# Optimization experiments

Hardware: AMD Instinct MI355X
Metric: run time of the kernel (lower is better)

The kernel has to match this reference:

```python
import jax, jax.numpy as jnp
import numpy as np

DEPTH = 4
CHUNK = 16


def tp(a, b):
    """Graded tensor (outer) product on flattened levels: (...,m)x(...,n)->(...,m*n)."""
    return jnp.einsum('...i,...j->...ij', a, b).reshape(*a.shape[:-1], a.shape[-1] * b.shape[-1])


def ta_mul(a, b):
    """Truncated tensor-algebra product of two group-like elements (implicit level-0 == 1).
    a, b: lists of levels 1..D, level k flattened to C**k."""
    out = []
    for k in range(len(a)):
        t = a[k] + b[k]
        for i in range(k):
            t = t + tp(a[i], b[k - 1 - i])
        out.append(t)
    return out


def ta_mulz(a, b):
    """Product when both elements have level-0 == 0."""
    out = []
    for k in range(len(a)):
        t = jnp.zeros_like(a[k])
        for i in range(k):
            t = t + tp(a[i], b[k - 1 - i])
        out.append(t)
    return out


def ta_exp(a):
    """exp of a level-0-free element, truncated at DEPTH; returns levels 1..D (level-0 == 1 implicit)."""
    out = list(a)
    p = a
    fact = 1.0
    for m in range(2, len(a) + 1):
        p = ta_mulz(a, p)
        fact *= m
        out = [o + q / fact for o, q in zip(out, p)]
    return out


def ta_log(s):
    """Truncated log of group-like element g = 1 + s; input s = levels 1..D of g."""
    out = list(s)
    p = s
    sign = 1.0
    for m in range(2, len(s) + 1):
        p = ta_mulz(s, p)
        sign = -sign
        out = [o + (sign / m) * q for o, q in zip(out, p)]
    return out


def bch(a, b):
    """BCH merge: log(exp(a) (x) exp(b)) in the truncated algebra."""
    return ta_log(ta_mul(ta_exp(a), ta_exp(b)))


def exp_l1(d):
    """exp of a pure level-1 element d (shape (...,C)): level k = d^(x)k / k!."""
    levels = [d]
    cur = d
    fact = 1.0
    for k in range(2, DEPTH + 1):
        cur = tp(cur, d)
        fact *= k
        levels.append(cur / fact)
    return levels


def chunk_signatures(inc):
    """inc: (B, N, L, C) per-chunk increments -> signature levels [(B,N,C), (B,N,C^2), ...]
    via Chen: sig = exp(d_1) (x) ... (x) exp(d_L)."""
    carry0 = tuple(exp_l1(inc[:, :, 0]))
    xs = jnp.moveaxis(inc[:, :, 1:], 2, 0)  # (L-1, B, N, C)
    def step(carry, d):
        return tuple(ta_mul(list(carry), exp_l1(d))), None
    carry, _ = jax.lax.scan(step, carry0, xs)
    return list(carry)


def hillis_steele(levels):
    """Inclusive associative scan over chunk dim (axis=1) with BCH merge.
    bch(0, b) == b exactly, so zero-padding handles the boundary."""
    N = levels[0].shape[1]
    pref = levels
    d = 1
    while d < N:
        shifted = [jnp.concatenate([jnp.zeros_like(l[:, :d]), l[:, :-d]], axis=1) for l in pref]
        pref = bch(shifted, pref)
        d *= 2
    return pref


def _forward(x, W1, b1, W2, b2):
    B, T, Cin = x.shape
    t = jnp.linspace(0.0, 1.0, T, dtype=x.dtype)
    path = jnp.concatenate([x, jnp.broadcast_to(t[None, :, None], (B, T, 1)).astype(x.dtype)], axis=-1)
    C = Cin + 1
    # basepoint=True: path starts at 0, so increments are diff of [0; path]
    inc = jnp.diff(path, axis=1, prepend=jnp.zeros((B, 1, C), x.dtype))
    N = T // CHUNK
    inc = inc.reshape(B, N, CHUNK, C)
    sig = chunk_signatures(inc)          # levels 1..D, (B,N,C^k)
    logl = ta_log(sig)                   # truncated log-signature per chunk
    pref = hillis_steele(logl)           # inclusive BCH prefix scan
    flat = jnp.concatenate(pref, axis=-1)  # (B, N, mem_dim)
    pooled = flat.mean(axis=1)           # readout_pool == 'mean'
    h = jnp.maximum(pooled @ W1 + b1, 0.0)
    return h @ W2 + b2


def setup_inputs() -> dict:
    key = jax.random.key(0)
    k0, k1, k2 = jax.random.split(key, 3)
    B, T, Cin = 8, 2048, 7
    mem_dim, H, out_dim = 4680, 256, 1
    x = jax.random.normal(k0, (B, T, Cin), dtype=jnp.float32)
    W1 = jax.random.normal(k1, (mem_dim, H), dtype=jnp.float32) * (1.0 / np.sqrt(mem_dim))
    b1 = jnp.zeros((H,), jnp.float32)
    W2 = jax.random.normal(k2, (H, out_dim), dtype=jnp.float32) * (1.0 / np.sqrt(H))
    b2 = jnp.zeros((out_dim,), jnp.float32)
    return {"x": x, "W1": W1, "b1": b1, "W2": W2, "b2": b2}


def reference(x, W1, b1, W2, b2):
    return _forward(x, W1, b1, W2, b2)
```

## Files before the change

kernel.cpp:

```cpp
#include <hip/hip_runtime.h>


#define MEM   4680
#define OFF2  8
#define OFF3  72
#define OFF4  584
#define NCH   128
#define NG    32
#define LCH   4
#define TLEN  2048
#define GSTR  20
#define ZN    (8 * MEM + 8 * 256)

__global__ __launch_bounds__(256) void group_sig_kernel(const float* __restrict__ x,
                                                        float* __restrict__ Q,
                                                        float* __restrict__ zbuf) {
    int blk = blockIdx.x;
    int b = blk >> 5, g = blk & 31;
    int tid = threadIdx.x;
    int lane = tid & 63, w = tid >> 6;
    int kq = lane >> 3, lq = lane & 7;

    for (int i = blk * 256 + tid; i < ZN; i += 256 * 256) zbuf[i] = 0.0f;

    __shared__ float sInc[64 * 8];
    __shared__ __attribute__((aligned(16))) float sG[512 * GSTR];
    __shared__ float sA[MEM];
    __shared__ float loc3[512];
    __shared__ float loc2[64];
    __shared__ float loc1[8];

    for (int e = tid; e < 64 * 8; e += 256) {
        int s = e >> 3, c = e & 7;
        int t = g * 64 + s;
        float v;
        if (c < 7) {
            float cur  = x[(b * TLEN + t) * 7 + c];
            float prev = (t > 0) ? x[(b * TLEN + t - 1) * 7 + c] : 0.0f;
            v = cur - prev;
        } else {
            v = (t > 0) ? (1.0f / 2047.0f) : 0.0f;
        }
        sInc[e] = v;
    }
    for (int m = tid; m < MEM; m += 256) sA[m] = 0.0f;
    __syncthreads();

    for (int c = 0; c < LCH; c++) {
        const float* dch = &sInc[c * 128];

        int pos1 = tid, pos2 = tid + 256;
        int i1 = pos1 >> 6, j1 = (pos1 >> 3) & 7, k1 = pos1 & 7;
        int i2 = pos2 >> 6;
        float p1a = 0.0f, l2a = 0.0f, l3a = 0.0f;
        float p1b = 0.0f, l2b = 0.0f, l3b = 0.0f;
        float ga[16], gb[16];
#pragma unroll
        for (int t = 0; t < 16; t++) {
            float di1 = dch[t * 8 + i1], di2 = dch[t * 8 + i2];
            float dj = dch[t * 8 + j1], dk = dch[t * 8 + k1];
            ga[t] = l3a + dk * (l2a * 0.5f + dj * (p1a * (1.0f / 6.0f) + di1 * (1.0f / 24.0f)));
            gb[t] = l3b + dk * (l2b * 0.5f + dj * (p1b * (1.0f / 6.0f) + di2 * (1.0f / 24.0f)));
            l3a += dk * (l2a + dj * (p1a * 0.5f + di1 * (1.0f / 6.0f)));
            l3b += dk * (l2b + dj * (p1b * 0.5f + di2 * (1.0f / 6.0f)));
            l2a += p1a * dj + di1 * dj * 0.5f;
            l2b += p1b * dj + di2 * dj * 0.5f;
            p1a += di1;
            p1b += di2;
        }
        {
            float4* gp1 = (float4*)&sG[pos1 * GSTR];
            float4* gp2 = (float4*)&sG[pos2 * GSTR];
            gp1[0] = make_float4(ga[0], ga[1], ga[2], ga[3]);
            gp1[1] = make_float4(ga[4], ga[5], ga[6], ga[7]);
            gp1[2] = make_float4(ga[8], ga[9], ga[10], ga[11]);
            gp1[3] = make_float4(ga[12], ga[13], ga[14], ga[15]);
            gp2[0] = make_float4(gb[0], gb[1], gb[2], gb[3]);
            gp2[1] = make_float4(gb[4], gb[5], gb[6], gb[7]);
            gp2[2] = make_float4(gb[8], gb[9], gb[10], gb[11]);
            gp2[3] = make_float4(gb[12], gb[13], gb[14], gb[15]);
        }
        loc3[pos1] = l3a;
        loc3[pos2] = l3b;
        if (k1 == 0) { loc2[pos1 >> 3] = l2a; loc2[pos2 >> 3] = l2b; }
        if ((pos1 & 63) == 0) { loc1[i1] = p1a; loc1[i2] = p1b; }
        __syncthreads();

        float dl[16];
#pragma unroll
        for (int t = 0; t < 16; t++) dl[t] = dch[t * 8 + lq];

        float r4[16];
#pragma unroll
        for (int r = 0; r < 16; r++) {
            int row = w + 4 * r;
            int i = row >> 3, j = row & 7;
            int m = row * 64 + lane;
            const float4* gp = (const float4*)&sG[(row * 8 + kq) * GSTR];
            float4 g0 = gp[0], g1 = gp[1], g2 = gp[2], g3 = gp[3];
            float acc = g0.x * dl[0] + g0.y * dl[1] + g0.z * dl[2] + g0.w * dl[3]
                      + g1.x * dl[4] + g1.y * dl[5] + g1.z * dl[6] + g1.w * dl[7]
                      + g2.x * dl[8] + g2.y * dl[9] + g2.z * dl[10] + g2.w * dl[11]
                      + g3.x * dl[12] + g3.y * dl[13] + g3.z * dl[14] + g3.w * dl[15];
            r4[r] = sA[OFF4 + m] + acc
                  + sA[i] * loc3[j * 64 + lane]
                  + sA[OFF2 + row] * loc2[lane]
                  + sA[OFF3 + row * 8 + kq] * loc1[lq];
        }
        float r3[2];
#pragma unroll
        for (int q = 0; q < 2; q++) {
            int m3 = tid + 256 * q;
            float l3v = (q == 0) ? l3a : l3b;
            r3[q] = sA[OFF3 + m3] + l3v
                  + sA[m3 >> 6] * loc2[m3 & 63]
                  + sA[OFF2 + (m3 >> 3)] * loc1[m3 & 7];
        }
        float r2v = 0.0f, r1v = 0.0f;
        if (tid < 64) r2v = sA[OFF2 + tid] + loc2[tid] + sA[tid >> 3] * loc1[tid & 7];
        if (tid < 8)  r1v = sA[tid] + loc1[tid];
        __syncthreads();

        size_t qbase = (size_t)(blk * LCH + c) * MEM;
#pragma unroll
        for (int r = 0; r < 16; r++) {
            int row = w + 4 * r;
            int m = row * 64 + lane;
            sA[OFF4 + m] = r4[r];
            Q[qbase + OFF4 + m] = r4[r];
        }
        sA[OFF3 + tid] = r3[0];       Q[qbase + OFF3 + tid] = r3[0];
        sA[OFF3 + 256 + tid] = r3[1]; Q[qbase + OFF3 + 256 + tid] = r3[1];
        if (tid < 64) { sA[OFF2 + tid] = r2v; Q[qbase + OFF2 + tid] = r2v; }
        if (tid < 8)  { sA[tid] = r1v;        Q[qbase + tid] = r1v; }
        __syncthreads();
    }
}

__global__ __launch_bounds__(256) void scan_fused_kernel(const float* __restrict__ Q,
                                                         float* __restrict__ P) {
    int bx = blockIdx.x;
    int b = bx >> 4, s = bx & 15;
    int tid = threadIdx.x;

    __shared__ float st1[NG][8];
    __shared__ float st2[NG][64];
    __shared__ float st3[NG][32];
    __shared__ float sp1[NG][8];
    __shared__ float sp2[NG][64];
    __shared__ float sp3[NG][32];

    {
        int g = tid >> 3, i = tid & 7;
        st1[g][i] = Q[((size_t)((b * NG + g) * LCH + 3)) * MEM + i];
    }
    for (int m = tid; m < NG * 64; m += 256) {
        int g = m >> 6, e = m & 63;
        st2[g][e] = Q[((size_t)((b * NG + g) * LCH + 3)) * MEM + OFF2 + e];
    }
    for (int m = tid; m < NG * 32; m += 256) {
        int g = m >> 5, e = m & 31;
        st3[g][e] = Q[((size_t)((b * NG + g) * LCH + 3)) * MEM + OFF3 + s * 32 + e];
    }
    __syncthreads();

    if (tid < 64) {
        int i = tid >> 3, k = tid & 7;
        float p1acc = 0.0f, p2acc = 0.0f;
        for (int g = 0; g < NG; g++) {
            sp2[g][tid] = p2acc;
            if (k == 0) sp1[g][i] = p1acc;
            if (s == 0) {
                size_t prow = (size_t)(b * NG + g) * MEM;
                P[prow + OFF2 + tid] = p2acc;
                if (k == 0) P[prow + i] = p1acc;
            }
            p2acc += st2[g][tid] + p1acc * st1[g][k];
            p1acc += st1[g][i];
        }
    }
    __syncthreads();

    if (tid < 32) {
        int ijk = s * 32 + tid;
        int i = ijk >> 6, jk = ijk & 63, ij = ijk >> 3, k = ijk & 7;
        float acc3 = 0.0f;
        for (int g = 0; g < NG; g++) {
            sp3[g][tid] = acc3;
            P[(size_t)(b * NG + g) * MEM + OFF3 + ijk] = acc3;
            acc3 += st3[g][tid] + sp1[g][i] * st2[g][jk] + sp2[g][ij] * st1[g][k];
        }
    }
    __syncthreads();

    int m = s * 256 + tid;
    int i = m >> 9, jkl = m & 511, ij = m >> 6, ijk_l = tid >> 3, kl = m & 63, l = m & 7;
    float acc4 = 0.0f;
#pragma unroll 4
    for (int g = 0; g < NG; g++) {
        size_t prow = (size_t)(b * NG + g) * MEM;
        size_t qrow = (size_t)((b * NG + g) * LCH + 3) * MEM;
        P[prow + OFF4 + m] = acc4;
        acc4 += Q[qrow + OFF4 + m]
              + sp1[g][i] * Q[qrow + OFF3 + jkl]
              + sp2[g][ij] * st2[g][kl]
              + sp3[g][ijk_l] * st1[g][l];
    }
}

__global__ __launch_bounds__(256) void apply_log_pool_kernel(const float* __restrict__ Q,
                                                             const float* __restrict__ P,
                                                             float* __restrict__ pooled) {
    int blk = blockIdx.x;
    int b = blk >> 5;
    int tid = threadIdx.x;
    int lane = tid & 63, w = tid >> 6;
    int kq = lane >> 3, lq = lane & 7;

    __shared__ float sA[MEM];
    __shared__ float sB[LCH * MEM];
    __shared__ float sR[OFF4];
    __shared__ float sP23[512];

    {
        const float4* srcP = (const float4*)(P + (size_t)blk * MEM);
        float4* dstA = (float4*)sA;
        for (int m = tid; m < MEM / 4; m += 256) dstA[m] = srcP[m];
        const float4* srcQ = (const float4*)(Q + (size_t)blk * LCH * MEM);
        float4* dstB = (float4*)sB;
        for (int m = tid; m < LCH * MEM / 4; m += 256) dstB[m] = srcQ[m];
    }
    __syncthreads();

    float pool4[16];
#pragma unroll
    for (int r = 0; r < 16; r++) pool4[r] = 0.0f;
    float pool3[2] = {0.0f, 0.0f};
    float pool2 = 0.0f, pool1 = 0.0f;

    for (int c = 0; c < LCH; c++) {
        const float* sBc = &sB[c * MEM];
        float b1l = sBc[lq];
        float b2lane = sBc[OFF2 + lane];

        float r1 = 0.0f, r2v = 0.0f;
        float r3v[2];
#pragma unroll
        for (int q = 0; q < 2; q++) {
            int m3 = tid + 256 * q;
            r3v[q] = sA[OFF3 + m3] + sBc[OFF3 + m3]
                   + sA[m3 >> 6] * sBc[OFF2 + (m3 & 63)]
                   + sA[OFF2 + (m3 >> 3)] * sBc[m3 & 7];
        }
        if (tid < 64) r2v = sA[OFF2 + tid] + sBc[OFF2 + tid] + sA[tid >> 3] * sBc[tid & 7];
        if (tid < 8)  r1 = sA[tid] + sBc[tid];

        float r4[16];
#pragma unroll
        for (int r = 0; r < 16; r++) {
            int row = w + 4 * r;
            int i = row >> 3, j = row & 7;
            int m = row * 64 + lane;
            r4[r] = sA[OFF4 + m] + sBc[OFF4 + m]
                  + sA[i] * sBc[OFF3 + j * 64 + lane]
                  + sA[OFF2 + row] * b2lane
                  + sA[OFF3 + row * 8 + kq] * b1l;
        }

        __syncthreads();
#pragma unroll
        for (int q = 0; q < 2; q++) sR[OFF3 + tid + 256 * q] = r3v[q];
        if (tid < 64) sR[OFF2 + tid] = r2v;
        if (tid < 8)  sR[tid] = r1;
        __syncthreads();

#pragma unroll
        for (int q = 0; q < 2; q++) {
            int m3 = tid + 256 * q;
            int i = m3 >> 6;
            sP23[m3] = sR[i] * sR[OFF2 + (m3 & 63)]
                     + sR[OFF2 + i * 8 + ((m3 >> 3) & 7)] * sR[m3 & 7];
        }
        __syncthreads();

        float s1l = sR[lq];
        float s2lane = sR[OFF2 + lane];
        float p22lane = sR[kq] * sR[lq];
#pragma unroll
        for (int r = 0; r < 16; r++) {
            int row = w + 4 * r;
            int i = row >> 3, j = row & 7;
            float s1i = sR[i];
            float p24 = s1i * sR[OFF3 + j * 64 + lane] + sR[OFF2 + row] * s2lane
                      + sR[OFF3 + row * 8 + kq] * s1l;
            float p34 = s1i * sP23[j * 64 + lane] + sR[OFF2 + row] * p22lane;
            float p44 = s1i * sR[j] * p22lane;
            pool4[r] += r4[r] - 0.5f * p24 + (1.0f / 3.0f) * p34 - 0.25f * p44;
        }
#pragma unroll
        for (int q = 0; q < 2; q++) {
            int m3 = tid + 256 * q;
            int i3 = m3 >> 6;
            pool3[q] += r3v[q] - 0.5f * sP23[m3] + (1.0f / 3.0f) * sR[i3] * p22lane;
        }
        if (tid < 64) pool2 += r2v - 0.5f * sR[tid >> 3] * sR[tid & 7];
        if (tid < 8)  pool1 += r1;
    }

    const float sc = 1.0f / (float)NCH;
    float* pb = pooled + (size_t)b * MEM;
#pragma unroll
    for (int r = 0; r < 16; r++) {
        int row = w + 4 * r;
        atomicAdd(&pb[OFF4 + row * 64 + lane], pool4[r] * sc);
    }
    atomicAdd(&pb[OFF3 + tid], pool3[0] * sc);
    atomicAdd(&pb[OFF3 + 256 + tid], pool3[1] * sc);
    if (tid < 64) atomicAdd(&pb[OFF2 + tid], pool2 * sc);
    if (tid < 8)  atomicAdd(&pb[tid], pool1 * sc);
}

__global__ __launch_bounds__(256) void gemv1_kernel(const float* __restrict__ pooled,
                                                    const float* __restrict__ W1,
                                                    float* __restrict__ hbuf) {
    int kc = blockIdx.x;
    int tid = threadIdx.x;
    int k0 = kc * 32;
    __shared__ float sp[8][32];
    {
        int b = tid >> 5, kk = tid & 31;
        sp[b][kk] = (k0 + kk < MEM) ? pooled[b * MEM + k0 + kk] : 0.0f;
    }
    __syncthreads();
    float acc[8];
#pragma unroll
    for (int b = 0; b < 8; b++) acc[b] = 0.0f;
    int kend = (k0 + 32 < MEM) ? (k0 + 32) : MEM;
    for (int k = k0; k < kend; k++) {
        float wv = W1[(size_t)k * 256 + tid];
#pragma unroll
        for (int b = 0; b < 8; b++) acc[b] += sp[b][k - k0] * wv;
    }
#pragma unroll
    for (int b = 0; b < 8; b++) atomicAdd(&hbuf[b * 256 + tid], acc[b]);
}

__global__ __launch_bounds__(256) void final_kernel(const float* __restrict__ hbuf,
                                                    const float* __restrict__ b1,
                                                    const float* __restrict__ W2,
                                                    const float* __restrict__ b2,
                                                    float* __restrict__ outp) {
    int b = blockIdx.x;
    int tid = threadIdx.x;
    float v = hbuf[b * 256 + tid] + b1[tid];
    v = fmaxf(v, 0.0f) * W2[tid];
    __shared__ float sRed[256];
    sRed[tid] = v;
    __syncthreads();
    for (int s = 128; s > 0; s >>= 1) {
        if (tid < s) sRed[tid] += sRed[tid + s];
        __syncthreads();
    }
    if (tid == 0) outp[b] = sRed[0] + b2[0];
}

extern "C" void kernel_launch(void* const* d_in, const int* in_sizes, int n_in,
                              void* d_out, int out_size, void* d_ws, size_t ws_size,
                              hipStream_t stream) {
    const float* x  = (const float*)d_in[0];
    const float* W1 = (const float*)d_in[1];
    const float* b1 = (const float*)d_in[2];
    const float* W2 = (const float*)d_in[3];
    const float* b2 = (const float*)d_in[4];
    float* out = (float*)d_out;

    float* ws = (float*)d_ws;
    float* Q      = ws;
    float* P      = Q + (size_t)1024 * MEM;
    float* pooled = P + (size_t)256 * MEM;
    float* hbuf   = pooled + 8 * MEM;

    group_sig_kernel<<<256, 256, 0, stream>>>(x, Q, pooled);
    scan_fused_kernel<<<128, 256, 0, stream>>>(Q, P);
    apply_log_pool_kernel<<<256, 256, 0, stream>>>(Q, P, pooled);
    gemv1_kernel<<<147, 256, 0, stream>>>(pooled, W1, hbuf);
    final_kernel<<<8, 256, 0, stream>>>(hbuf, b1, W2, b2, out);
}
```

Before: 127.5 us.

## Recompute per-chunk signatures in pool kernel instead of storing all to global

The first kernel now writes only the group-total signature per 64-step group instead of all four intermediate chunk prefix signatures, which shrinks the workspace traffic. The apply/pool kernel reloads the increments and recomputes the chunk prefix signatures on the fly. Level-4 accumulation is also restructured so each thread owns 8 contiguous l-entries, with running sums over l in registers and no staged G buffer in shared memory. This trades duplicated signature compute for fewer global writes and reads.

```diff
diff --git a/kernel.cpp b/kernel.cpp
--- a/kernel.cpp
+++ b/kernel.cpp
@@ -2,142 +2,106 @@
 
 
 #define MEM   4680
-#define OFF2  8
-#define OFF3  72
-#define OFF4  584
-#define NCH   128
+#define L2OFF 8
+#define L3OFF 72
+#define L4OFF 584
 #define NG    32
-#define LCH   4
 #define TLEN  2048
-#define GSTR  20
 #define ZN    (8 * MEM + 8 * 256)
 
-__global__ __launch_bounds__(256) void group_sig_kernel(const float* __restrict__ x,
-                                                        float* __restrict__ Q,
-                                                        float* __restrict__ zbuf) {
-    int blk = blockIdx.x;
-    int b = blk >> 5, g = blk & 31;
-    int tid = threadIdx.x;
-    int lane = tid & 63, w = tid >> 6;
-    int kq = lane >> 3, lq = lane & 7;
-
-    for (int i = blk * 256 + tid; i < ZN; i += 256 * 256) zbuf[i] = 0.0f;
-
-    __shared__ float sInc[64 * 8];
-    __shared__ __attribute__((aligned(16))) float sG[512 * GSTR];
-    __shared__ float sA[MEM];
-    __shared__ float loc3[512];
-    __shared__ float loc2[64];
-    __shared__ float loc1[8];
-
-    for (int e = tid; e < 64 * 8; e += 256) {
+__device__ __forceinline__ void load_inc(const float* __restrict__ x, int b, int g,
+                                         float* sInc, int tid) {
+    for (int e = tid; e < 512; e += 256) {
         int s = e >> 3, c = e & 7;
         int t = g * 64 + s;
         float v;
         if (c < 7) {
             float cur  = x[(b * TLEN + t) * 7 + c];
-            float prev = (t > 0) ? x[(b * TLEN + t - 1) * 7 + c] : 0.0f;
+            float prev = (t > 0) ? x[(b * TLEN + t - 1) * 7 + c] : 0.f;
             v = cur - prev;
-        } else {
-            v = (t > 0) ? (1.0f / 2047.0f) : 0.0f;
-        }
+        } else v = (t > 0) ? (1.f / 2047.f) : 0.f;
         sInc[e] = v;
     }
-    for (int m = tid; m < MEM; m += 256) sA[m] = 0.0f;
-    __syncthreads();
-
-    for (int c = 0; c < LCH; c++) {
-        const float* dch = &sInc[c * 128];
-
-        int pos1 = tid, pos2 = tid + 256;
-        int i1 = pos1 >> 6, j1 = (pos1 >> 3) & 7, k1 = pos1 & 7;
-        int i2 = pos2 >> 6;
-        float p1a = 0.0f, l2a = 0.0f, l3a = 0.0f;
-        float p1b = 0.0f, l2b = 0.0f, l3b = 0.0f;
-        float ga[16], gb[16];
-#pragma unroll
-        for (int t = 0; t < 16; t++) {
-            float di1 = dch[t * 8 + i1], di2 = dch[t * 8 + i2];
-            float dj = dch[t * 8 + j1], dk = dch[t * 8 + k1];
-            ga[t] = l3a + dk * (l2a * 0.5f + dj * (p1a * (1.0f / 6.0f) + di1 * (1.0f / 24.0f)));
-            gb[t] = l3b + dk * (l2b * 0.5f + dj * (p1b * (1.0f / 6.0f) + di2 * (1.0f / 24.0f)));
-            l3a += dk * (l2a + dj * (p1a * 0.5f + di1 * (1.0f / 6.0f)));
-            l3b += dk * (l2b + dj * (p1b * 0.5f + di2 * (1.0f / 6.0f)));
-            l2a += p1a * dj + di1 * dj * 0.5f;
-            l2b += p1b * dj + di2 * dj * 0.5f;
-            p1a += di1;
-            p1b += di2;
-        }
-        {
-            float4* gp1 = (float4*)&sG[pos1 * GSTR];
-            float4* gp2 = (float4*)&sG[pos2 * GSTR];
-            gp1[0] = make_float4(ga[0], ga[1], ga[2], ga[3]);
-            gp1[1] = make_float4(ga[4], ga[5], ga[6], ga[7]);
-            gp1[2] = make_float4(ga[8], ga[9], ga[10], ga[11]);
-            gp1[3] = make_float4(ga[12], ga[13], ga[14], ga[15]);
-            gp2[0] = make_float4(gb[0], gb[1], gb[2], gb[3]);
-            gp2[1] = make_float4(gb[4], gb[5], gb[6], gb[7]);
-            gp2[2] = make_float4(gb[8], gb[9], gb[10], gb[11]);
-            gp2[3] = make_float4(gb[12], gb[13], gb[14], gb[15]);
-        }
-        loc3[pos1] = l3a;
-        loc3[pos2] = l3b;
-        if (k1 == 0) { loc2[pos1 >> 3] = l2a; loc2[pos2 >> 3] = l2b; }
-        if ((pos1 & 63) == 0) { loc1[i1] = p1a; loc1[i2] = p1b; }
-        __syncthreads();
-
-        float dl[16];
-#pragma unroll
-        for (int t = 0; t < 16; t++) dl[t] = dch[t * 8 + lq];
-
-        float r4[16];
-#pragma unroll
-        for (int r = 0; r < 16; r++) {
-            int row = w + 4 * r;
-            int i = row >> 3, j = row & 7;
-            int m = row * 64 + lane;
-            const float4* gp = (const float4*)&sG[(row * 8 + kq) * GSTR];
-            float4 g0 = gp[0], g1 = gp[1], g2 = gp[2], g3 = gp[3];
-            float acc = g0.x * dl[0] + g0.y * dl[1] + g0.z * dl[2] + g0.w * dl[3]
-                      + g1.x * dl[4] + g1.y * dl[5] + g1.z * dl[6] + g1.w * dl[7]
-                      + g2.x * dl[8] + g2.y * dl[9] + g2.z * dl[10] + g2.w * dl[11]
-                      + g3.x * dl[12] + g3.y * dl[13] + g3.z * dl[14] + g3.w * dl[15];
-            r4[r] = sA[OFF4 + m] + acc
-                  + sA[i] * loc3[j * 64 + lane]
-                  + sA[OFF2 + row] * loc2[lane]
-                  + sA[OFF3 + row * 8 + kq] * loc1[lq];
-        }
-        float r3[2];
-#pragma unroll
-        for (int q = 0; q < 2; q++) {
-            int m3 = tid + 256 * q;
-            float l3v = (q == 0) ? l3a : l3b;
-            r3[q] = sA[OFF3 + m3] + l3v
-                  + sA[m3 >> 6] * loc2[m3 & 63]
-                  + sA[OFF2 + (m3 >> 3)] * loc1[m3 & 7];
-        }
-        float r2v = 0.0f, r1v = 0.0f;
-        if (tid < 64) r2v = sA[OFF2 + tid] + loc2[tid] + sA[tid >> 3] * loc1[tid & 7];
-        if (tid < 8)  r1v = sA[tid] + loc1[tid];
-        __syncthreads();
-
-        size_t qbase = (size_t)(blk * LCH + c) * MEM;
-#pragma unroll
-        for (int r = 0; r < 16; r++) {
-            int row = w + 4 * r;
-            int m = row * 64 + lane;
-            sA[OFF4 + m] = r4[r];
-            Q[qbase + OFF4 + m] = r4[r];
-        }
-        sA[OFF3 + tid] = r3[0];       Q[qbase + OFF3 + tid] = r3[0];
-        sA[OFF3 + 256 + tid] = r3[1]; Q[qbase + OFF3 + 256 + tid] = r3[1];
-        if (tid < 64) { sA[OFF2 + tid] = r2v; Q[qbase + OFF2 + tid] = r2v; }
-        if (tid < 8)  { sA[tid] = r1v;        Q[qbase + tid] = r1v; }
-        __syncthreads();
-    }
-}
-
-__global__ __launch_bounds__(256) void scan_fused_kernel(const float* __restrict__ Q,
+}
+
+__device__ __forceinline__ void chunk_step(const float* dch, float* sA, float* U, int tid) {
+    float* loc3 = U;
+    float* loc2 = U + 512;
+    float* loc1 = U + 576;
+    const int i1 = tid >> 6, j1 = (tid >> 3) & 7, k1 = tid & 7;
+    const int pos2 = tid + 256, i2 = pos2 >> 6;
+    float p1a = 0.f, l2a = 0.f, l3a = 0.f, p1b = 0.f, l2b = 0.f, l3b = 0.f;
+    float Sa[8], Sb[8];
+#pragma unroll
+    for (int l = 0; l < 8; l++) { Sa[l] = 0.f; Sb[l] = 0.f; }
+#pragma unroll
+    for (int t = 0; t < 16; t++) {
+        const float* dr = dch + t * 8;
+        float di1 = dr[i1], di2 = dr[i2], dj = dr[j1], dk = dr[k1];
+        float ga = l3a + dk * (l2a * 0.5f + dj * (p1a * (1.f/6.f) + di1 * (1.f/24.f)));
+        float gb = l3b + dk * (l2b * 0.5f + dj * (p1b * (1.f/6.f) + di2 * (1.f/24.f)));
+#pragma unroll
+        for (int l = 0; l < 8; l++) { float dv = dr[l]; Sa[l] += ga * dv; Sb[l] += gb * dv; }
+        l3a += dk * (l2a + dj * (p1a * 0.5f + di1 * (1.f/6.f)));
+        l3b += dk * (l2b + dj * (p1b * 0.5f + di2 * (1.f/6.f)));
+        l2a += (p1a + di1 * 0.5f) * dj;
+        l2b += (p1b + di2 * 0.5f) * dj;
+        p1a += di1; p1b += di2;
+    }
+    loc3[tid] = l3a; loc3[pos2] = l3b;
+    if (k1 == 0) { loc2[tid >> 3] = l2a; loc2[(tid >> 3) + 32] = l2b; }
+    if ((tid & 63) == 0) { loc1[i1] = p1a; loc1[i2] = p1b; }
+    __syncthreads();
+    float n4a[8], n4b[8];
+    {
+        float a1 = sA[i1], a2 = sA[L2OFF + (tid >> 3)], a3 = sA[L3OFF + tid];
+        float c1_ = sA[i2], c2_ = sA[L2OFF + (tid >> 3) + 32], c3_ = sA[L3OFF + pos2];
+        const float* l3p = &loc3[(tid & 63) * 8];
+        const float* l2p = &loc2[k1 * 8];
+#pragma unroll
+        for (int l = 0; l < 8; l++) {
+            float v3 = l3p[l], v2 = l2p[l], v1 = loc1[l];
+            n4a[l] = sA[L4OFF + tid * 8 + l]  + Sa[l] + a1 * v3 + a2 * v2 + a3 * v1;
+            n4b[l] = sA[L4OFF + pos2 * 8 + l] + Sb[l] + c1_ * v3 + c2_ * v2 + c3_ * v1;
+        }
+    }
+    float n3a = sA[L3OFF + tid]  + l3a + sA[i1] * loc2[tid & 63] + sA[L2OFF + (tid >> 3)] * loc1[k1];
+    float n3b = sA[L3OFF + pos2] + l3b + sA[i2] * loc2[tid & 63] + sA[L2OFF + (tid >> 3) + 32] * loc1[k1];
+    float n2v = 0.f, n1v = 0.f;
+    if (tid < 64) n2v = sA[L2OFF + tid] + loc2[tid] + sA[tid >> 3] * loc1[tid & 7];
+    if (tid < 8)  n1v = sA[tid] + loc1[tid];
+    __syncthreads();
+#pragma unroll
+    for (int l = 0; l < 8; l++) { sA[L4OFF + tid * 8 + l] = n4a[l]; sA[L4OFF + pos2 * 8 + l] = n4b[l]; }
+    sA[L3OFF + tid] = n3a; sA[L3OFF + pos2] = n3b;
+    if (tid < 64) sA[L2OFF + tid] = n2v;
+    if (tid < 8)  sA[tid] = n1v;
+    __syncthreads();
+}
+
+__global__ __launch_bounds__(256) void sig_totals_kernel(const float* __restrict__ x,
+                                                         float* __restrict__ T,
+                                                         float* __restrict__ zbuf) {
+    int blk = blockIdx.x;
+    int b = blk >> 5, g = blk & 31;
+    int tid = threadIdx.x;
+
+    for (int i = blk * 256 + tid; i < ZN; i += 256 * 256) zbuf[i] = 0.f;
+
+    __shared__ __attribute__((aligned(16))) float sInc[512];
+    __shared__ __attribute__((aligned(16))) float sA[MEM];
+    __shared__ __attribute__((aligned(16))) float U[584];
+
+    load_inc(x, b, g, sInc, tid);
+    for (int m = tid; m < MEM; m += 256) sA[m] = 0.f;
+    __syncthreads();
+    for (int c = 0; c < 4; c++) chunk_step(&sInc[c * 128], sA, U, tid);
+    const float4* s4 = (const float4*)sA;
+    float4* t4 = (float4*)(T + (size_t)blk * MEM);
+    for (int m = tid; m < MEM / 4; m += 256) t4[m] = s4[m];
+}
+
+__global__ __launch_bounds__(256) void scan_fused_kernel(const float* __restrict__ T,
                                                          float* __restrict__ P) {
     int bx = blockIdx.x;
     int b = bx >> 4, s = bx & 15;
@@ -150,29 +114,30 @@
     __shared__ float sp2[NG][64];
     __shared__ float sp3[NG][32];
 
+    int bBase = b * NG;
     {
         int g = tid >> 3, i = tid & 7;
-        st1[g][i] = Q[((size_t)((b * NG + g) * LCH + 3)) * MEM + i];
+        st1[g][i] = T[(size_t)(bBase + g) * MEM + i];
     }
     for (int m = tid; m < NG * 64; m += 256) {
         int g = m >> 6, e = m & 63;
-        st2[g][e] = Q[((size_t)((b * NG + g) * LCH + 3)) * MEM + OFF2 + e];
+        st2[g][e] = T[(size_t)(bBase + g) * MEM + L2OFF + e];
     }
     for (int m = tid; m < NG * 32; m += 256) {
         int g = m >> 5, e = m & 31;
-        st3[g][e] = Q[((size_t)((b * NG + g) * LCH + 3)) * MEM + OFF3 + s * 32 + e];
+        st3[g][e] = T[(size_t)(bBase + g) * MEM + L3OFF + s * 32 + e];
     }
     __syncthreads();
 
     if (tid < 64) {
         int i = tid >> 3, k = tid & 7;
-        float p1acc = 0.0f, p2acc = 0.0f;
+        float p1acc = 0.f, p2acc = 0.f;
         for (int g = 0; g < NG; g++) {
             sp2[g][tid] = p2acc;
             if (k == 0) sp1[g][i] = p1acc;
             if (s == 0) {
-                size_t prow = (size_t)(b * NG + g) * MEM;
-                P[prow + OFF2 + tid] = p2acc;
+                size_t prow = (size_t)(bBase + g) * MEM;
+                P[prow + L2OFF + tid] = p2acc;
                 if (k == 0) P[prow + i] = p1acc;
             }
             p2acc += st2[g][tid] + p1acc * st1[g][k];
@@ -180,144 +145,130 @@
         }
     }
     __syncthreads();
-
     if (tid < 32) {
         int ijk = s * 32 + tid;
         int i = ijk >> 6, jk = ijk & 63, ij = ijk >> 3, k = ijk & 7;
-        float acc3 = 0.0f;
+        float acc3 = 0.f;
         for (int g = 0; g < NG; g++) {
             sp3[g][tid] = acc3;
-            P[(size_t)(b * NG + g) * MEM + OFF3 + ijk] = acc3;
+            P[(size_t)(bBase + g) * MEM + L3OFF + ijk] = acc3;
             acc3 += st3[g][tid] + sp1[g][i] * st2[g][jk] + sp2[g][ij] * st1[g][k];
         }
     }
     __syncthreads();
-
-    int m = s * 256 + tid;
-    int i = m >> 9, jkl = m & 511, ij = m >> 6, ijk_l = tid >> 3, kl = m & 63, l = m & 7;
-    float acc4 = 0.0f;
+    {
+        int m = s * 256 + tid;
+        int i = m >> 9, jkl = m & 511, ij = m >> 6, kl = m & 63, l = m & 7;
+        int p3loc = tid >> 3;
+        float acc4 = 0.f;
 #pragma unroll 4
-    for (int g = 0; g < NG; g++) {
-        size_t prow = (size_t)(b * NG + g) * MEM;
-        size_t qrow = (size_t)((b * NG + g) * LCH + 3) * MEM;
-        P[prow + OFF4 + m] = acc4;
-        acc4 += Q[qrow + OFF4 + m]
-              + sp1[g][i] * Q[qrow + OFF3 + jkl]
-              + sp2[g][ij] * st2[g][kl]
-              + sp3[g][ijk_l] * st1[g][l];
-    }
-}
-
-__global__ __launch_bounds__(256) void apply_log_pool_kernel(const float* __restrict__ Q,
+        for (int g = 0; g < NG; g++) {
+            size_t row = (size_t)(bBase + g) * MEM;
+            P[row + L4OFF + m] = acc4;
+            acc4 += T[row + L4OFF + m]
+                  + sp1[g][i] * T[row + L3OFF + jkl]
+                  + sp2[g][ij] * st2[g][kl]
+                  + sp3[g][p3loc] * st1[g][l];
+        }
+    }
+}
+
+__global__ __launch_bounds__(256) void apply_log_pool_kernel(const float* __restrict__ x,
                                                              const float* __restrict__ P,
                                                              float* __restrict__ pooled) {
     int blk = blockIdx.x;
-    int b = blk >> 5;
-    int tid = threadIdx.x;
-    int lane = tid & 63, w = tid >> 6;
-    int kq = lane >> 3, lq = lane & 7;
-
-    __shared__ float sA[MEM];
-    __shared__ float sB[LCH * MEM];
-    __shared__ float sR[OFF4];
-    __shared__ float sP23[512];
-
-    {
-        const float4* srcP = (const float4*)(P + (size_t)blk * MEM);
-        float4* dstA = (float4*)sA;
-        for (int m = tid; m < MEM / 4; m += 256) dstA[m] = srcP[m];
-        const float4* srcQ = (const float4*)(Q + (size_t)blk * LCH * MEM);
-        float4* dstB = (float4*)sB;
-        for (int m = tid; m < LCH * MEM / 4; m += 256) dstB[m] = srcQ[m];
-    }
-    __syncthreads();
-
-    float pool4[16];
-#pragma unroll
-    for (int r = 0; r < 16; r++) pool4[r] = 0.0f;
-    float pool3[2] = {0.0f, 0.0f};
-    float pool2 = 0.0f, pool1 = 0.0f;
-
-    for (int c = 0; c < LCH; c++) {
-        const float* sBc = &sB[c * MEM];
-        float b1l = sBc[lq];
-        float b2lane = sBc[OFF2 + lane];
-
-        float r1 = 0.0f, r2v = 0.0f;
-        float r3v[2];
-#pragma unroll
-        for (int q = 0; q < 2; q++) {
-            int m3 = tid + 256 * q;
-            r3v[q] = sA[OFF3 + m3] + sBc[OFF3 + m3]
-                   + sA[m3 >> 6] * sBc[OFF2 + (m3 & 63)]
-                   + sA[OFF2 + (m3 >> 3)] * sBc[m3 & 7];
-        }
-        if (tid < 64) r2v = sA[OFF2 + tid] + sBc[OFF2 + tid] + sA[tid >> 3] * sBc[tid & 7];
-        if (tid < 8)  r1 = sA[tid] + sBc[tid];
-
-        float r4[16];
-#pragma unroll
-        for (int r = 0; r < 16; r++) {
-            int row = w + 4 * r;
-            int i = row >> 3, j = row & 7;
-            int m = row * 64 + lane;
-            r4[r] = sA[OFF4 + m] + sBc[OFF4 + m]
-                  + sA[i] * sBc[OFF3 + j * 64 + lane]
-                  + sA[OFF2 + row] * b2lane
-                  + sA[OFF3 + row * 8 + kq] * b1l;
-        }
-
+    int b = blk >> 5, g = blk & 31;
+    int tid = threadIdx.x;
+
+    __shared__ __attribute__((aligned(16))) float sInc[512];
+    __shared__ __attribute__((aligned(16))) float sA[MEM];
+    __shared__ __attribute__((aligned(16))) float sP[MEM];
+    __shared__ __attribute__((aligned(16))) float U[1680];
+
+    load_inc(x, b, g, sInc, tid);
+    {
+        const float4* p4 = (const float4*)(P + (size_t)blk * MEM);
+        float4* sp4 = (float4*)sP;
+        for (int m = tid; m < MEM / 4; m += 256) sp4[m] = p4[m];
+    }
+    for (int m = tid; m < MEM; m += 256) sA[m] = 0.f;
+    __syncthreads();
+
+    const int i1 = tid >> 6, j1 = (tid >> 3) & 7, k1 = tid & 7;
+    const int pos2 = tid + 256, i2 = pos2 >> 6;
+    float pool4a[8], pool4b[8];
+#pragma unroll
+    for (int l = 0; l < 8; l++) { pool4a[l] = 0.f; pool4b[l] = 0.f; }
+    float pool3a = 0.f, pool3b = 0.f, pool2 = 0.f, pool1 = 0.f;
+    float* sR = U + 584;
+    float* sQ23 = U + 1168;
+
+    for (int c = 0; c < 4; c++) {
+        chunk_step(&sInc[c * 128], sA, U, tid);
+        float R4a[8], R4b[8];
+        {
+            float a1 = sP[i1], a2 = sP[L2OFF + (tid >> 3)], a3 = sP[L3OFF + tid];
+            float c1_ = sP[i2], c2_ = sP[L2OFF + (tid >> 3) + 32], c3_ = sP[L3OFF + pos2];
+            const float* q3p = &sA[L3OFF + (tid & 63) * 8];
+            const float* q2p = &sA[L2OFF + k1 * 8];
+#pragma unroll
+            for (int l = 0; l < 8; l++) {
+                float v3 = q3p[l], v2 = q2p[l], v1 = sA[l];
+                R4a[l] = sP[L4OFF + tid * 8 + l]  + sA[L4OFF + tid * 8 + l]  + a1 * v3 + a2 * v2 + a3 * v1;
+                R4b[l] = sP[L4OFF + pos2 * 8 + l] + sA[L4OFF + pos2 * 8 + l] + c1_ * v3 + c2_ * v2 + c3_ * v1;
+            }
+        }
+        float R3a = sP[L3OFF + tid]  + sA[L3OFF + tid]  + sP[i1] * sA[L2OFF + (tid & 63)] + sP[L2OFF + (tid >> 3)] * sA[k1];
+        float R3b = sP[L3OFF + pos2] + sA[L3OFF + pos2] + sP[i2] * sA[L2OFF + (tid & 63)] + sP[L2OFF + (tid >> 3) + 32] * sA[k1];
+        float R2v = 0.f, R1v = 0.f;
+        if (tid < 64) R2v = sP[L2OFF + tid] + sA[L2OFF + tid] + sP[tid >> 3] * sA[tid & 7];
+        if (tid < 8)  R1v = sP[tid] + sA[tid];
+        sR[72 + tid] = R3a; sR[72 + pos2] = R3b;
+        if (tid < 64) sR[8 + tid] = R2v;
+        if (tid < 8)  sR[tid] = R1v;
         __syncthreads();
-#pragma unroll
-        for (int q = 0; q < 2; q++) sR[OFF3 + tid + 256 * q] = r3v[q];
-        if (tid < 64) sR[OFF2 + tid] = r2v;
-        if (tid < 8)  sR[tid] = r1;
+        sQ23[tid]  = sR[tid >> 6] * sR[8 + (tid & 63)] + sR[8 + (tid >> 3)] * sR[tid & 7];
+        sQ23[pos2] = sR[pos2 >> 6] * sR[8 + (tid & 63)] + sR[8 + (tid >> 3) + 32] * sR[tid & 7];
         __syncthreads();
-
-#pragma unroll
-        for (int q = 0; q < 2; q++) {
-            int m3 = tid + 256 * q;
-            int i = m3 >> 6;
-            sP23[m3] = sR[i] * sR[OFF2 + (m3 & 63)]
-                     + sR[OFF2 + i * 8 + ((m3 >> 3) & 7)] * sR[m3 & 7];
+        {
+            float s1ia = sR[i1], s1ib = sR[i2], s1j = sR[j1], s1k = sR[k1];
+            float s2ija = sR[8 + (tid >> 3)], s2ijb = sR[8 + (tid >> 3) + 32];
+            const float* r3p = &sR[72 + (tid & 63) * 8];
+            const float* r2p = &sR[8 + k1 * 8];
+            const float* q23p = &sQ23[(tid & 63) * 8];
+#pragma unroll
+            for (int l = 0; l < 8; l++) {
+                float s1l = sR[l];
+                float p22 = s1k * s1l;
+                float p24a = s1ia * r3p[l] + s2ija * r2p[l] + R3a * s1l;
+                float p24b = s1ib * r3p[l] + s2ijb * r2p[l] + R3b * s1l;
+                float p34a = s1ia * q23p[l] + s2ija * p22;
+                float p34b = s1ib * q23p[l] + s2ijb * p22;
+                float p44a = s1ia * s1j * p22;
+                float p44b = s1ib * s1j * p22;
+                pool4a[l] += R4a[l] - 0.5f * p24a + (1.f/3.f) * p34a - 0.25f * p44a;
+                pool4b[l] += R4b[l] - 0.5f * p24b + (1.f/3.f) * p34b - 0.25f * p44b;
+            }
+            pool3a += R3a - 0.5f * sQ23[tid]  + (1.f/3.f) * s1ia * s1j * s1k;
+            pool3b += R3b - 0.5f * sQ23[pos2] + (1.f/3.f) * s1ib * s1j * s1k;
+            if (tid < 64) pool2 += R2v - 0.5f * sR[tid >> 3] * sR[tid & 7];
+            if (tid < 8)  pool1 += R1v;
         }
         __syncthreads();
-
-        float s1l = sR[lq];
-        float s2lane = sR[OFF2 + lane];
-        float p22lane = sR[kq] * sR[lq];
-#pragma unroll
-        for (int r = 0; r < 16; r++) {
-            int row = w + 4 * r;
-            int i = row >> 3, j = row & 7;
-            float s1i = sR[i];
-            float p24 = s1i * sR[OFF3 + j * 64 + lane] + sR[OFF2 + row] * s2lane
-                      + sR[OFF3 + row * 8 + kq] * s1l;
-            float p34 = s1i * sP23[j * 64 + lane] + sR[OFF2 + row] * p22lane;
-            float p44 = s1i * sR[j] * p22lane;
-            pool4[r] += r4[r] - 0.5f * p24 + (1.0f / 3.0f) * p34 - 0.25f * p44;
-        }
-#pragma unroll
-        for (int q = 0; q < 2; q++) {
-            int m3 = tid + 256 * q;
-            int i3 = m3 >> 6;
-            pool3[q] += r3v[q] - 0.5f * sP23[m3] + (1.0f / 3.0f) * sR[i3] * p22lane;
-        }
-        if (tid < 64) pool2 += r2v - 0.5f * sR[tid >> 3] * sR[tid & 7];
-        if (tid < 8)  pool1 += r1;
-    }
-
-    const float sc = 1.0f / (float)NCH;
-    float* pb = pooled + (size_t)b * MEM;
-#pragma unroll
-    for (int r = 0; r < 16; r++) {
-        int row = w + 4 * r;
-        atomicAdd(&pb[OFF4 + row * 64 + lane], pool4[r] * sc);
-    }
-    atomicAdd(&pb[OFF3 + tid], pool3[0] * sc);
-    atomicAdd(&pb[OFF3 + 256 + tid], pool3[1] * sc);
-    if (tid < 64) atomicAdd(&pb[OFF2 + tid], pool2 * sc);
-    if (tid < 8)  atomicAdd(&pb[tid], pool1 * sc);
+    }
+    {
+        const float sc = 1.f / 128.f;
+        float* pb = pooled + (size_t)b * MEM;
+#pragma unroll
+        for (int l = 0; l < 8; l++) {
+            atomicAdd(&pb[L4OFF + tid * 8 + l],  pool4a[l] * sc);
+            atomicAdd(&pb[L4OFF + pos2 * 8 + l], pool4b[l] * sc);
+        }
+        atomicAdd(&pb[L3OFF + tid],  pool3a * sc);
+        atomicAdd(&pb[L3OFF + pos2], pool3b * sc);
+        if (tid < 64) atomicAdd(&pb[L2OFF + tid], pool2 * sc);
+        if (tid < 8)  atomicAdd(&pb[tid], pool1 * sc);
+    }
 }
 
 __global__ __launch_bounds__(256) void gemv1_kernel(const float* __restrict__ pooled,
@@ -329,12 +280,12 @@
     __shared__ float sp[8][32];
     {
         int b = tid >> 5, kk = tid & 31;
-        sp[b][kk] = (k0 + kk < MEM) ? pooled[b * MEM + k0 + kk] : 0.0f;
+        sp[b][kk] = (k0 + kk < MEM) ? pooled[b * MEM + k0 + kk] : 0.f;
     }
     __syncthreads();
     float acc[8];
 #pragma unroll
-    for (int b = 0; b < 8; b++) acc[b] = 0.0f;
+    for (int b = 0; b < 8; b++) acc[b] = 0.f;
     int kend = (k0 + 32 < MEM) ? (k0 + 32) : MEM;
     for (int k = k0; k < kend; k++) {
         float wv = W1[(size_t)k * 256 + tid];
@@ -353,7 +304,7 @@
     int b = blockIdx.x;
     int tid = threadIdx.x;
     float v = hbuf[b * 256 + tid] + b1[tid];
-    v = fmaxf(v, 0.0f) * W2[tid];
+    v = fmaxf(v, 0.f) * W2[tid];
     __shared__ float sRed[256];
     sRed[tid] = v;
     __syncthreads();
@@ -375,14 +326,14 @@
     float* out = (float*)d_out;
 
     float* ws = (float*)d_ws;
-    float* Q      = ws;
-    float* P      = Q + (size_t)1024 * MEM;
+    float* T      = ws;
+    float* P      = T + (size_t)256 * MEM;
     float* pooled = P + (size_t)256 * MEM;
     float* hbuf   = pooled + 8 * MEM;
 
-    group_sig_kernel<<<256, 256, 0, stream>>>(x, Q, pooled);
-    scan_fused_kernel<<<128, 256, 0, stream>>>(Q, P);
-    apply_log_pool_kernel<<<256, 256, 0, stream>>>(Q, P, pooled);
+    sig_totals_kernel<<<256, 256, 0, stream>>>(x, T, pooled);
+    scan_fused_kernel<<<128, 256, 0, stream>>>(T, P);
+    apply_log_pool_kernel<<<256, 256, 0, stream>>>(x, P, pooled);
     gemv1_kernel<<<147, 256, 0, stream>>>(pooled, W1, hbuf);
     final_kernel<<<8, 256, 0, stream>>>(hbuf, b1, W2, b2, out);
 }
```

Result: slower. 152.0 us (+19.2%).
